# Performance work log

Measured on AMD Instinct MI355X. Metric: run time of the kernel, lower is better.

The kernel has to match this reference:

```python
import jax, jax.numpy as jnp
import numpy as np

B, L_Q, L_K = 16, 256, 256
Q_DIM, K_DIM, H_DIM, V_DIM = 256, 256, 128, 128


def setup_inputs() -> dict:
    key = jax.random.key(0)
    k1, k2, k3, k4, k5, k6 = jax.random.split(key, 6)
    query = jax.random.normal(k1, (B, L_Q, Q_DIM), dtype=jnp.float32)
    key_t = jax.random.normal(k2, (B, L_K, K_DIM), dtype=jnp.float32)
    value = jax.random.normal(k3, (B, L_Q, V_DIM), dtype=jnp.float32)
    # Linear weights stored as [in, out] for x @ W (equivalent to torch Linear, no bias)
    Wq = jax.random.normal(k4, (Q_DIM, H_DIM), dtype=jnp.float32) / np.sqrt(Q_DIM)
    Wk = jax.random.normal(k5, (K_DIM, H_DIM), dtype=jnp.float32) / np.sqrt(K_DIM)
    v = jax.random.uniform(k6, (H_DIM,), dtype=jnp.float32, minval=-0.1, maxval=0.1)
    return {"query": query, "key": key_t, "value": value, "Wq": Wq, "Wk": Wk, "v": v}


def reference(query, key, value, Wq, Wk, v):
    # Project first (equivalent to applying Linear after the expand, but cheaper):
    qp = jnp.einsum("bqd,dh->bqh", query, Wq)  # [B, l_q, h]
    kp = jnp.einsum("bkd,dh->bkh", key, Wk)    # [B, l_k, h]
    # score[b, k, q] = tanh(qp[b,q] + kp[b,k]) . v  -> [B, l_k, l_q]
    score = jnp.einsum("bkqh,h->bkq", jnp.tanh(qp[:, None, :, :] + kp[:, :, None, :]), v)
    attention = jax.nn.softmax(score, axis=-1)  # softmax over query positions (dim -1)
    context = jnp.einsum("bkq,bqv->bkv", attention, value)  # bmm
    return context, attention
```

## Files before the change

kernel.cpp:

```cpp
#include <hip/hip_runtime.h>

#define B_  16
#define LQ  256
#define LK  256
#define QD  256
#define HD  128
#define VD  128

#define SCALE2 2.8853900817779268f
#define L2E    1.4426950408889634f
#define CTX_SIZE (B_ * LK * VD)

__device__ __forceinline__ float fast_exp2(float x) { return __builtin_amdgcn_exp2f(x); }
__device__ __forceinline__ float fast_rcp(float x)  { return __builtin_amdgcn_rcpf(x); }

__global__ __launch_bounds__(256) void proj_kernel(const float* __restrict__ query,
                                                   const float* __restrict__ key,
                                                   const float* __restrict__ Wq,
                                                   const float* __restrict__ Wk,
                                                   float* __restrict__ qe_t,
                                                   float* __restrict__ ke)
{
    __shared__ float  Xs[8][260];
    __shared__ float4 part[4][8][32];

    const int t = threadIdx.x;
    const bool isQ = (blockIdx.x < 512);
    const int blk  = isQ ? blockIdx.x : (blockIdx.x - 512);
    const int rows0 = blk * 8;
    const float* X = isQ ? query : key;
    const float* W = isQ ? Wq : Wk;

    {
        const int r = t >> 5;
        const int c = (t & 31) * 8;
        const float4 x0 = *(const float4*)(X + (size_t)(rows0 + r) * QD + c);
        const float4 x1 = *(const float4*)(X + (size_t)(rows0 + r) * QD + c + 4);
        *(float4*)&Xs[r][c]     = x0;
        *(float4*)&Xs[r][c + 4] = x1;
    }
    __syncthreads();

    const int w    = t >> 6;
    const int lane = t & 63;
    const int hg   = lane & 31;
    const int mb   = lane >> 5;

    float4 acc[4];
#pragma unroll
    for (int i = 0; i < 4; i++) acc[i] = make_float4(0.f, 0.f, 0.f, 0.f);

    const int kbase = w * 64;
#pragma unroll 4
    for (int kk = 0; kk < 64; kk++) {
        const int k = kbase + kk;
        const float4 wv = *(const float4*)(W + (size_t)k * HD + hg * 4);
#pragma unroll
        for (int mi = 0; mi < 4; mi++) {
            const float xv = Xs[mb + mi * 2][k];
            acc[mi].x += xv * wv.x;
            acc[mi].y += xv * wv.y;
            acc[mi].z += xv * wv.z;
            acc[mi].w += xv * wv.w;
        }
    }
#pragma unroll
    for (int mi = 0; mi < 4; mi++) part[w][mb + mi * 2][hg] = acc[mi];
    __syncthreads();

    {
        const int m   = t >> 5;
        const int hg2 = t & 31;
        float4 s = part[0][m][hg2];
        const float4 p1 = part[1][m][hg2];
        const float4 p2 = part[2][m][hg2];
        const float4 p3 = part[3][m][hg2];
        s.x += p1.x + p2.x + p3.x;
        s.y += p1.y + p2.y + p3.y;
        s.z += p1.z + p2.z + p3.z;
        s.w += p1.w + p2.w + p3.w;
        float4 e = make_float4(fast_exp2(s.x * SCALE2), fast_exp2(s.y * SCALE2),
                               fast_exp2(s.z * SCALE2), fast_exp2(s.w * SCALE2));
        const int row = rows0 + m;
        if (isQ) {
            const int b = row >> 8, q = row & 255;
            float* base = qe_t + ((size_t)b * HD + hg2 * 4) * LQ + q;
            base[0 * LQ] = e.x;
            base[1 * LQ] = e.y;
            base[2 * LQ] = e.z;
            base[3 * LQ] = e.w;
        } else {
            *(float4*)(ke + (size_t)row * HD + hg2 * 4) = e;
        }
    }
}

__global__ __launch_bounds__(256) void attn_kernel(const float* __restrict__ qe_t,
                                                   const float* __restrict__ ke,
                                                   const float* __restrict__ v,
                                                   const float* __restrict__ value,
                                                   float* __restrict__ out)
{
    __shared__ float  score_s[4][260];
    __shared__ float  attn_T[256][4];
    __shared__ float2 partc[4][4][64];

    const int t  = threadIdx.x;
    const int b  = blockIdx.x >> 6;
    const int k0 = (blockIdx.x & 63) << 2;

    const float* qeb = qe_t + (size_t)b * HD * LQ;
    const float* keb = ke + ((size_t)b * LK + k0) * HD;

    float acc0 = 0.f, acc1 = 0.f, acc2 = 0.f, acc3 = 0.f;
    const int q = t;
#pragma unroll 2
    for (int h0 = 0; h0 < HD; h0 += 8) {
        float qv[8];
#pragma unroll
        for (int j = 0; j < 8; j++) qv[j] = qeb[(size_t)(h0 + j) * LQ + q];
#pragma unroll
        for (int j = 0; j < 8; j++) {
            const float vh = v[h0 + j];
            acc0 += vh * fast_rcp(qv[j] * keb[0 * HD + h0 + j] + 1.0f);
            acc1 += vh * fast_rcp(qv[j] * keb[1 * HD + h0 + j] + 1.0f);
            acc2 += vh * fast_rcp(qv[j] * keb[2 * HD + h0 + j] + 1.0f);
            acc3 += vh * fast_rcp(qv[j] * keb[3 * HD + h0 + j] + 1.0f);
        }
    }
    float sumv = 0.f;
#pragma unroll
    for (int h = 0; h < HD; h++) sumv += v[h];

    score_s[0][q] = sumv - 2.f * acc0;
    score_s[1][q] = sumv - 2.f * acc1;
    score_s[2][q] = sumv - 2.f * acc2;
    score_s[3][q] = sumv - 2.f * acc3;
    __syncthreads();

    const int w = t >> 6, lane = t & 63;
    {
        float x0 = score_s[w][lane];
        float x1 = score_s[w][lane + 64];
        float x2 = score_s[w][lane + 128];
        float x3 = score_s[w][lane + 192];
        float m = fmaxf(fmaxf(x0, x1), fmaxf(x2, x3));
#pragma unroll
        for (int off = 32; off >= 1; off >>= 1) m = fmaxf(m, __shfl_xor(m, off));
        float e0 = fast_exp2((x0 - m) * L2E);
        float e1 = fast_exp2((x1 - m) * L2E);
        float e2 = fast_exp2((x2 - m) * L2E);
        float e3 = fast_exp2((x3 - m) * L2E);
        float s = e0 + e1 + e2 + e3;
#pragma unroll
        for (int off = 32; off >= 1; off >>= 1) s += __shfl_xor(s, off);
        const float rs = fast_rcp(s);
        e0 *= rs; e1 *= rs; e2 *= rs; e3 *= rs;
        attn_T[lane][w]       = e0;
        attn_T[lane + 64][w]  = e1;
        attn_T[lane + 128][w] = e2;
        attn_T[lane + 192][w] = e3;
        float* ao = out + CTX_SIZE + ((size_t)(b * LK + k0 + w)) * LQ;
        ao[lane]       = e0;
        ao[lane + 64]  = e1;
        ao[lane + 128] = e2;
        ao[lane + 192] = e3;
    }
    __syncthreads();

    {
        const int vd2 = lane * 2;
        const float* valb = value + (size_t)b * LQ * VD;
        float2 c0 = {0.f, 0.f}, c1 = {0.f, 0.f}, c2 = {0.f, 0.f}, c3 = {0.f, 0.f};
#pragma unroll 4
        for (int i = 0; i < 64; i++) {
            const int q2 = (w << 6) + i;
            const float4 a = *(const float4*)&attn_T[q2][0];
            const float2 vv = *(const float2*)(valb + (size_t)q2 * VD + vd2);
            c0.x += a.x * vv.x; c0.y += a.x * vv.y;
            c1.x += a.y * vv.x; c1.y += a.y * vv.y;
            c2.x += a.z * vv.x; c2.y += a.z * vv.y;
            c3.x += a.w * vv.x; c3.y += a.w * vv.y;
        }
        partc[w][0][lane] = c0;
        partc[w][1][lane] = c1;
        partc[w][2][lane] = c2;
        partc[w][3][lane] = c3;
    }
    __syncthreads();
    {
        const int kg = t >> 6, l2 = t & 63;
        const float2 p0 = partc[0][kg][l2];
        const float2 p1 = partc[1][kg][l2];
        const float2 p2 = partc[2][kg][l2];
        const float2 p3 = partc[3][kg][l2];
        float2 s;
        s.x = p0.x + p1.x + p2.x + p3.x;
        s.y = p0.y + p1.y + p2.y + p3.y;
        *(float2*)(out + ((size_t)(b * LK + k0 + kg)) * VD + l2 * 2) = s;
    }
}

extern "C" void kernel_launch(void* const* d_in, const int* in_sizes, int n_in,
                              void* d_out, int out_size, void* d_ws, size_t ws_size,
                              hipStream_t stream)
{
    const float* query = (const float*)d_in[0];
    const float* key   = (const float*)d_in[1];
    const float* value = (const float*)d_in[2];
    const float* Wq    = (const float*)d_in[3];
    const float* Wk    = (const float*)d_in[4];
    const float* v     = (const float*)d_in[5];
    float* out = (float*)d_out;

    float* qe_t = (float*)d_ws;
    float* kew  = qe_t + (size_t)B_ * HD * LQ;

    proj_kernel<<<dim3(1024), 256, 0, stream>>>(query, key, Wq, Wk, qe_t, kew);
    attn_kernel<<<dim3(1024), 256, 0, stream>>>(qe_t, kew, v, value, out);
}
```

Measured before the change: 106.1 us.

## Store projected exp(2q) in h4-interleaved float4 layout and vectorize loads

Changes the workspace layout of the exponentiated query projection from [b][h][q] scalars to [b][h/4][q] float4, so the attention kernel loads four h values per thread in one 16-byte access. Key projections and v are also read as float4. The projection kernel's partial-sum buffer is transposed so the Q path can write float4s, and the inner loop reads two k values per step. Launch bounds gain a minimum of four blocks per CU, which may constrain register allocation.

```diff
diff --git a/kernel.cpp b/kernel.cpp
--- a/kernel.cpp
+++ b/kernel.cpp
@@ -14,22 +14,22 @@
 __device__ __forceinline__ float fast_exp2(float x) { return __builtin_amdgcn_exp2f(x); }
 __device__ __forceinline__ float fast_rcp(float x)  { return __builtin_amdgcn_rcpf(x); }
 
-__global__ __launch_bounds__(256) void proj_kernel(const float* __restrict__ query,
-                                                   const float* __restrict__ key,
-                                                   const float* __restrict__ Wq,
-                                                   const float* __restrict__ Wk,
-                                                   float* __restrict__ qe_t,
-                                                   float* __restrict__ ke)
+__global__ __launch_bounds__(256, 4) void proj_kernel(const float* __restrict__ query,
+                                                      const float* __restrict__ key,
+                                                      const float* __restrict__ Wq,
+                                                      const float* __restrict__ Wk,
+                                                      float4* __restrict__ qe4,
+                                                      float4* __restrict__ ke4)
 {
-    __shared__ float  Xs[8][260];
-    __shared__ float4 part[4][8][32];
+    __shared__ float  Xs[8][258];
+    __shared__ float4 part[4][32][9];
 
     const int t = threadIdx.x;
     const bool isQ = (blockIdx.x < 512);
     const int blk  = isQ ? blockIdx.x : (blockIdx.x - 512);
     const int rows0 = blk * 8;
     const float* X = isQ ? query : key;
-    const float* W = isQ ? Wq : Wk;
+    const float4* W4 = (const float4*)(isQ ? Wq : Wk);
 
     {
         const int r = t >> 5;
@@ -52,54 +52,54 @@
 
     const int kbase = w * 64;
 #pragma unroll 4
-    for (int kk = 0; kk < 64; kk++) {
+    for (int kk = 0; kk < 64; kk += 2) {
         const int k = kbase + kk;
-        const float4 wv = *(const float4*)(W + (size_t)k * HD + hg * 4);
+        const float4 w0 = W4[(size_t)k * 32 + hg];
+        const float4 w1 = W4[(size_t)(k + 1) * 32 + hg];
 #pragma unroll
         for (int mi = 0; mi < 4; mi++) {
-            const float xv = Xs[mb + mi * 2][k];
-            acc[mi].x += xv * wv.x;
-            acc[mi].y += xv * wv.y;
-            acc[mi].z += xv * wv.z;
-            acc[mi].w += xv * wv.w;
+            const float2 x = *(const float2*)&Xs[mb + 2 * mi][k];
+            acc[mi].x += x.x * w0.x + x.y * w1.x;
+            acc[mi].y += x.x * w0.y + x.y * w1.y;
+            acc[mi].z += x.x * w0.z + x.y * w1.z;
+            acc[mi].w += x.x * w0.w + x.y * w1.w;
         }
     }
 #pragma unroll
-    for (int mi = 0; mi < 4; mi++) part[w][mb + mi * 2][hg] = acc[mi];
-    __syncthreads();
-
-    {
-        const int m   = t >> 5;
-        const int hg2 = t & 31;
-        float4 s = part[0][m][hg2];
-        const float4 p1 = part[1][m][hg2];
-        const float4 p2 = part[2][m][hg2];
-        const float4 p3 = part[3][m][hg2];
-        s.x += p1.x + p2.x + p3.x;
-        s.y += p1.y + p2.y + p3.y;
-        s.z += p1.z + p2.z + p3.z;
-        s.w += p1.w + p2.w + p3.w;
-        float4 e = make_float4(fast_exp2(s.x * SCALE2), fast_exp2(s.y * SCALE2),
-                               fast_exp2(s.z * SCALE2), fast_exp2(s.w * SCALE2));
-        const int row = rows0 + m;
-        if (isQ) {
-            const int b = row >> 8, q = row & 255;
-            float* base = qe_t + ((size_t)b * HD + hg2 * 4) * LQ + q;
-            base[0 * LQ] = e.x;
-            base[1 * LQ] = e.y;
-            base[2 * LQ] = e.z;
-            base[3 * LQ] = e.w;
-        } else {
-            *(float4*)(ke + (size_t)row * HD + hg2 * 4) = e;
-        }
+    for (int mi = 0; mi < 4; mi++) part[w][hg][mb + 2 * mi] = acc[mi];
+    __syncthreads();
+
+    if (isQ) {
+        const int q8 = t & 7, h4 = t >> 3;
+        float4 s = part[0][h4][q8];
+        const float4 p1 = part[1][h4][q8];
+        const float4 p2 = part[2][h4][q8];
+        const float4 p3 = part[3][h4][q8];
+        s.x += p1.x + p2.x + p3.x;  s.y += p1.y + p2.y + p3.y;
+        s.z += p1.z + p2.z + p3.z;  s.w += p1.w + p2.w + p3.w;
+        const float4 e = make_float4(fast_exp2(s.x * SCALE2), fast_exp2(s.y * SCALE2),
+                                     fast_exp2(s.z * SCALE2), fast_exp2(s.w * SCALE2));
+        const int row = rows0 + q8, b = row >> 8, q = row & 255;
+        qe4[((size_t)b * 32 + h4) * 256 + q] = e;
+    } else {
+        const int h4 = t & 31, m = t >> 5;
+        float4 s = part[0][h4][m];
+        const float4 p1 = part[1][h4][m];
+        const float4 p2 = part[2][h4][m];
+        const float4 p3 = part[3][h4][m];
+        s.x += p1.x + p2.x + p3.x;  s.y += p1.y + p2.y + p3.y;
+        s.z += p1.z + p2.z + p3.z;  s.w += p1.w + p2.w + p3.w;
+        const float4 e = make_float4(fast_exp2(s.x * SCALE2), fast_exp2(s.y * SCALE2),
+                                     fast_exp2(s.z * SCALE2), fast_exp2(s.w * SCALE2));
+        ke4[(size_t)(rows0 + m) * 32 + h4] = e;
     }
 }
 
-__global__ __launch_bounds__(256) void attn_kernel(const float* __restrict__ qe_t,
-                                                   const float* __restrict__ ke,
-                                                   const float* __restrict__ v,
-                                                   const float* __restrict__ value,
-                                                   float* __restrict__ out)
+__global__ __launch_bounds__(256, 4) void attn_kernel(const float4* __restrict__ qe4,
+                                                      const float4* __restrict__ ke4,
+                                                      const float* __restrict__ v,
+                                                      const float* __restrict__ value,
+                                                      float* __restrict__ out)
 {
     __shared__ float  score_s[4][260];
     __shared__ float  attn_T[256][4];
@@ -109,28 +109,35 @@
     const int b  = blockIdx.x >> 6;
     const int k0 = (blockIdx.x & 63) << 2;
 
-    const float* qeb = qe_t + (size_t)b * HD * LQ;
-    const float* keb = ke + ((size_t)b * LK + k0) * HD;
+    const float4* qb = qe4 + (size_t)b * 32 * 256;
+    const float4* kb = ke4 + ((size_t)b * LK + k0) * 32;
+    const float4* v4 = (const float4*)v;
 
     float acc0 = 0.f, acc1 = 0.f, acc2 = 0.f, acc3 = 0.f;
     const int q = t;
-#pragma unroll 2
-    for (int h0 = 0; h0 < HD; h0 += 8) {
-        float qv[8];
-#pragma unroll
-        for (int j = 0; j < 8; j++) qv[j] = qeb[(size_t)(h0 + j) * LQ + q];
-#pragma unroll
-        for (int j = 0; j < 8; j++) {
-            const float vh = v[h0 + j];
-            acc0 += vh * fast_rcp(qv[j] * keb[0 * HD + h0 + j] + 1.0f);
-            acc1 += vh * fast_rcp(qv[j] * keb[1 * HD + h0 + j] + 1.0f);
-            acc2 += vh * fast_rcp(qv[j] * keb[2 * HD + h0 + j] + 1.0f);
-            acc3 += vh * fast_rcp(qv[j] * keb[3 * HD + h0 + j] + 1.0f);
-        }
+#pragma unroll 4
+    for (int h4 = 0; h4 < 32; h4++) {
+        const float4 qv = qb[(size_t)h4 * 256 + q];
+        const float4 vv = v4[h4];
+        const float4 ka = kb[0 * 32 + h4];
+        const float4 kc = kb[1 * 32 + h4];
+        const float4 kd = kb[2 * 32 + h4];
+        const float4 kf = kb[3 * 32 + h4];
+        acc0 += vv.x * fast_rcp(qv.x * ka.x + 1.f) + vv.y * fast_rcp(qv.y * ka.y + 1.f)
+              + vv.z * fast_rcp(qv.z * ka.z + 1.f) + vv.w * fast_rcp(qv.w * ka.w + 1.f);
+        acc1 += vv.x * fast_rcp(qv.x * kc.x + 1.f) + vv.y * fast_rcp(qv.y * kc.y + 1.f)
+              + vv.z * fast_rcp(qv.z * kc.z + 1.f) + vv.w * fast_rcp(qv.w * kc.w + 1.f);
+        acc2 += vv.x * fast_rcp(qv.x * kd.x + 1.f) + vv.y * fast_rcp(qv.y * kd.y + 1.f)
+              + vv.z * fast_rcp(qv.z * kd.z + 1.f) + vv.w * fast_rcp(qv.w * kd.w + 1.f);
+        acc3 += vv.x * fast_rcp(qv.x * kf.x + 1.f) + vv.y * fast_rcp(qv.y * kf.y + 1.f)
+              + vv.z * fast_rcp(qv.z * kf.z + 1.f) + vv.w * fast_rcp(qv.w * kf.w + 1.f);
     }
     float sumv = 0.f;
 #pragma unroll
-    for (int h = 0; h < HD; h++) sumv += v[h];
+    for (int h4 = 0; h4 < 32; h4++) {
+        const float4 vv = v4[h4];
+        sumv += vv.x + vv.y + vv.z + vv.w;
+    }
 
     score_s[0][q] = sumv - 2.f * acc0;
     score_s[1][q] = sumv - 2.f * acc1;
@@ -213,9 +220,9 @@
     const float* v     = (const float*)d_in[5];
     float* out = (float*)d_out;
 
-    float* qe_t = (float*)d_ws;
-    float* kew  = qe_t + (size_t)B_ * HD * LQ;
-
-    proj_kernel<<<dim3(1024), 256, 0, stream>>>(query, key, Wq, Wk, qe_t, kew);
-    attn_kernel<<<dim3(1024), 256, 0, stream>>>(qe_t, kew, v, value, out);
+    float4* qe4 = (float4*)d_ws;
+    float4* ke4 = qe4 + (size_t)B_ * 32 * 256;
+
+    proj_kernel<<<dim3(1024), 256, 0, stream>>>(query, key, Wq, Wk, qe4, ke4);
+    attn_kernel<<<dim3(1024), 256, 0, stream>>>(qe4, ke4, v, value, out);
 }
```

Result: slower. 109.1 us (+2.8%).
